# Kernel tuning notes

Hardware: AMD Instinct MI355X
Metric: run time of the kernel (lower is better)

## Reference

```python
import jax, jax.numpy as jnp
import numpy as np
from jax import lax

K_SIZE = 3
STRIDE = 1
PAD = 1
BN_EPS = 1e-5


def _unfold(x, k, stride, pad):
    # x: [B, C, H, W] -> patches [B, L, C*k*k] with torch.unfold feature
    # ordering (channel-major: feat = c*k*k + i*k + j), L = oH*oW
    B, C, H, W = x.shape
    xp = jnp.pad(x, ((0, 0), (0, 0), (pad, pad), (pad, pad)))
    oH = (H + 2 * pad - k) // stride + 1
    oW = (W + 2 * pad - k) // stride + 1
    views = []
    for i in range(k):
        for j in range(k):
            views.append(xp[:, :, i:i + oH * stride:stride, j:j + oW * stride:stride])
    p = jnp.stack(views, axis=0)            # [k*k, B, C, oH, oW]
    p = p.transpose(1, 3, 4, 2, 0)          # [B, oH, oW, C, k*k]
    return p.reshape(B, oH * oW, C * k * k), oH, oW


def _nearest_l1(flat, cents):
    # Online nearest-centroid search under L1, avoids [N, K] x D blowup.
    # flat: [N, D], cents: [K, D] -> int32 indices [N] (first min on ties,
    # matching torch argmin)
    N = flat.shape[0]
    init = (jnp.full((N,), jnp.inf, flat.dtype), jnp.zeros((N,), jnp.int32))
    ks = jnp.arange(cents.shape[0], dtype=jnp.int32)

    def body(carry, kc):
        kidx, c = kc
        d = jnp.abs(flat - c).sum(-1)       # [N]
        bd, bi = carry
        better = d < bd
        return (jnp.where(better, d, bd), jnp.where(better, kidx, bi)), None

    (_, best_idx), _ = lax.scan(body, init, (ks, cents))
    return best_idx


def setup_inputs() -> dict:
    key = jax.random.key(0)
    ks = jax.random.split(key, 5)
    B, Cin, H, W = 8, 64, 56, 56
    K, D, Cout = 256, Cin * K_SIZE * K_SIZE, 128
    return {
        "x": jax.random.normal(ks[0], (B, Cin, H, W), jnp.float32),
        "centroids": jax.random.normal(ks[1], (K, D), jnp.float32),
        "residual_centroids": jax.random.normal(ks[2], (K, D), jnp.float32),
        "dot_centroids": jax.random.normal(ks[3], (K, Cout), jnp.float32),
        "dot_residual_centroids": jax.random.normal(ks[4], (K, Cout), jnp.float32),
        "bn_gamma": jnp.ones((Cout,), jnp.float32),
        "bn_beta": jnp.zeros((Cout,), jnp.float32),
    }


def reference(x, centroids, residual_centroids, dot_centroids,
              dot_residual_centroids, bn_gamma, bn_beta):
    B = x.shape[0]
    Cout = dot_centroids.shape[1]
    patches, oH, oW = _unfold(x, K_SIZE, STRIDE, PAD)   # [B, L, D]
    L, D = patches.shape[1], patches.shape[2]
    flat = patches.reshape(B * L, D)

    # Stage 1: nearest centroid (L1)
    idx1 = _nearest_l1(flat, centroids)                  # [B*L]
    residuals = flat - centroids[idx1]                   # [B*L, D]
    # Stage 2: nearest residual centroid (L1)
    idx2 = _nearest_l1(residuals, residual_centroids)    # [B*L]

    # LUT gather + sum
    out_vals = dot_centroids[idx1] + dot_residual_centroids[idx2]  # [B*L, Cout]
    out = out_vals.reshape(B, L, Cout).transpose(0, 2, 1).reshape(B, Cout, oH, oW)

    # BatchNorm2d (training mode: biased batch statistics)
    mean = out.mean(axis=(0, 2, 3), keepdims=True)
    var = ((out - mean) ** 2).mean(axis=(0, 2, 3), keepdims=True)
    out = (out - mean) * lax.rsqrt(var + BN_EPS)
    out = out * bn_gamma[None, :, None, None] + bn_beta[None, :, None, None]
    return out
```

## Files before the change

### kernel.cpp

```cpp
#include <hip/hip_runtime.h>

#define NP 25088
#define DD 576
#define KC 256

__global__ __launch_bounds__(256) void unfold_kernel(const float* __restrict__ x,
                                                     float* __restrict__ PT) {
  const int d = blockIdx.y;
  const int n = blockIdx.x * 256 + threadIdx.x;
  const int c = d / 9, r = d % 9;
  const int di = r / 3 - 1, dj = r % 3 - 1;
  const int b = n / 3136, hw = n % 3136;
  const int h = hw / 56 + di, w = hw % 56 + dj;
  float v = 0.0f;
  if (h >= 0 && h < 56 && w >= 0 && w < 56)
    v = x[(((size_t)b * 64 + c) * 56 + h) * 56 + w];
  PT[(size_t)d * NP + n] = v;
}

__global__ __launch_bounds__(256) void transpose_kernel(const float* __restrict__ C,
                                                        float* __restrict__ CT) {
  const int d = blockIdx.x;
  const int k = threadIdx.x;
  CT[d * KC + k] = C[k * DD + d];
}

__global__ __launch_bounds__(256, 3) void nearest_kernel(const float* __restrict__ AT,
                                                         const float* __restrict__ CT,
                                                         float* __restrict__ distc,
                                                         int* __restrict__ idxc) {
  __shared__ float As[2][32][64];
  __shared__ float Bs[2][32][128];

  const int tid = threadIdx.x;
  const int tm = tid >> 4;
  const int tk = tid & 15;
  const int m0 = blockIdx.x * 64;
  const int kc = blockIdx.y;

  float part[4][8], tot[4][8];
  float4 ra[2], rb[4];

#define LOADT(ch) do {                                                              \
    _Pragma("unroll")                                                               \
    for (int q = 0; q < 2; ++q) {                                                   \
      int f = q * 256 + tid;                                                        \
      ra[q] = *(const float4*)(AT + (size_t)((ch) * 32 + (f >> 4)) * NP + m0 +      \
                               (f & 15) * 4);                                       \
    }                                                                               \
    _Pragma("unroll")                                                               \
    for (int q = 0; q < 4; ++q) {                                                   \
      int f = q * 256 + tid;                                                        \
      rb[q] = *(const float4*)(CT + (size_t)((ch) * 32 + (f >> 5)) * KC +           \
                               kc * 128 + (f & 31) * 4);                            \
    }                                                                               \
  } while (0)

#define WRITET(bf) do {                                                             \
    _Pragma("unroll")                                                               \
    for (int q = 0; q < 2; ++q) {                                                   \
      int f = q * 256 + tid;                                                        \
      *(float4*)&As[bf][f >> 4][(f & 15) * 4] = ra[q];                              \
    }                                                                               \
    _Pragma("unroll")                                                               \
    for (int q = 0; q < 4; ++q) {                                                   \
      int f = q * 256 + tid;                                                        \
      *(float4*)&Bs[bf][f >> 5][(f & 31) * 4] = rb[q];                              \
    }                                                                               \
  } while (0)

  LOADT(0);
  WRITET(0);
#pragma unroll
  for (int i = 0; i < 4; ++i)
#pragma unroll
    for (int j = 0; j < 8; ++j) tot[i][j] = 0.0f;

  for (int ch = 0; ch < 18; ++ch) {
    if ((ch & 1) == 0) {
#pragma unroll
      for (int i = 0; i < 4; ++i)
#pragma unroll
        for (int j = 0; j < 8; ++j) part[i][j] = 0.0f;
    }
    __syncthreads();
    if (ch < 17) LOADT(ch + 1);
    const int buf = ch & 1;
#pragma unroll 4
    for (int d = 0; d < 32; ++d) {
      float a[4], b[8];
      *(float4*)&a[0] = *(const float4*)&As[buf][d][tm * 4];
      *(float4*)&b[0] = *(const float4*)&Bs[buf][d][tk * 4];
      *(float4*)&b[4] = *(const float4*)&Bs[buf][d][64 + tk * 4];
#pragma unroll
      for (int i = 0; i < 4; ++i)
#pragma unroll
        for (int j = 0; j < 8; ++j) part[i][j] += fabsf(a[i] - b[j]);
    }
    if (ch < 17) WRITET((ch + 1) & 1);
    if (ch & 1) {
#pragma unroll
      for (int i = 0; i < 4; ++i)
#pragma unroll
        for (int j = 0; j < 8; ++j) tot[i][j] += part[i][j];
    }
  }

#pragma unroll
  for (int i = 0; i < 4; ++i) {
    float bd = tot[i][0];
    int bk = kc * 128 + tk * 4;
#pragma unroll
    for (int j = 1; j < 8; ++j) {
      int kk = kc * 128 + (j < 4 ? tk * 4 + j : 64 + tk * 4 + (j - 4));
      if (tot[i][j] < bd) { bd = tot[i][j]; bk = kk; }
    }
#pragma unroll
    for (int off = 1; off < 16; off <<= 1) {
      float od = __shfl_xor(bd, off, 64);
      int ok = __shfl_xor(bk, off, 64);
      if (od < bd || (od == bd && ok < bk)) { bd = od; bk = ok; }
    }
    if (tk == 0) {
      const int m = m0 + tm * 4 + i;
      distc[(size_t)kc * NP + m] = bd;
      idxc[(size_t)kc * NP + m] = bk;
    }
  }
#undef LOADT
#undef WRITET
}

__global__ __launch_bounds__(256) void combine_kernel(const float* __restrict__ distc,
                                                      const int* __restrict__ idxc,
                                                      int* __restrict__ idx_out) {
  const int n = blockIdx.x * 256 + threadIdx.x;
  if (n >= NP) return;
  const float d0 = distc[n], d1 = distc[NP + n];
  idx_out[n] = (d1 < d0) ? idxc[NP + n] : idxc[n];
}

__global__ __launch_bounds__(256) void resid_kernel(float* __restrict__ PT,
                                                    const float* __restrict__ C1T,
                                                    const int* __restrict__ idx1) {
  const int d = blockIdx.y;
  const int n = blockIdx.x * 256 + threadIdx.x;
  const int k = idx1[n];
  PT[(size_t)d * NP + n] -= C1T[d * KC + k];
}

__global__ __launch_bounds__(256) void stats_kernel(const int* __restrict__ idx1,
                                                    const int* __restrict__ idx2,
                                                    const float* __restrict__ dotc,
                                                    const float* __restrict__ dotrc,
                                                    float* __restrict__ gsum,
                                                    float* __restrict__ gsq) {
  __shared__ float ssum[4][128], ssq[4][128];
  const int tid = threadIdx.x, lane = tid & 63, wv = tid >> 6;
  const int wid = blockIdx.x * 4 + wv;
  float s0 = 0.f, s1 = 0.f, q0 = 0.f, q1 = 0.f;
  for (int n = wid; n < NP; n += 512) {
    const int k1 = idx1[n], k2 = idx2[n];
    const float2 u = ((const float2*)(dotc + (size_t)k1 * 128))[lane];
    const float2 v = ((const float2*)(dotrc + (size_t)k2 * 128))[lane];
    const float x0 = u.x + v.x, x1 = u.y + v.y;
    s0 += x0; s1 += x1; q0 += x0 * x0; q1 += x1 * x1;
  }
  ssum[wv][lane * 2] = s0; ssum[wv][lane * 2 + 1] = s1;
  ssq[wv][lane * 2] = q0;  ssq[wv][lane * 2 + 1] = q1;
  __syncthreads();
  if (tid < 128) {
    const float s = ssum[0][tid] + ssum[1][tid] + ssum[2][tid] + ssum[3][tid];
    const float q = ssq[0][tid] + ssq[1][tid] + ssq[2][tid] + ssq[3][tid];
    atomicAdd(&gsum[tid], s);
    atomicAdd(&gsq[tid], q);
  }
}

__global__ void finalize_kernel(const float* __restrict__ gsum,
                                const float* __restrict__ gsq,
                                const float* __restrict__ gamma,
                                const float* __restrict__ beta,
                                float* __restrict__ scalev,
                                float* __restrict__ shiftv) {
  const int c = threadIdx.x;
  const float mean = gsum[c] * (1.0f / NP);
  const float var = gsq[c] * (1.0f / NP) - mean * mean;
  const float inv = rsqrtf(var + 1e-5f);
  const float sc = gamma[c] * inv;
  scalev[c] = sc;
  shiftv[c] = beta[c] - mean * sc;
}

__global__ __launch_bounds__(256) void output_kernel(const int* __restrict__ idx1,
                                                     const int* __restrict__ idx2,
                                                     const float* __restrict__ dotc,
                                                     const float* __restrict__ dotrc,
                                                     const float* __restrict__ scalev,
                                                     const float* __restrict__ shiftv,
                                                     float* __restrict__ out) {
  __shared__ float vals[64][128];
  const int tid = threadIdx.x, lane = tid & 63, wv = tid >> 6;
  const int blk = blockIdx.x;
  const int b = blk / 49, hw0 = (blk % 49) * 64;
  const int n0 = b * 3136 + hw0;
  const float sc0 = scalev[lane * 2], sc1 = scalev[lane * 2 + 1];
  const float sh0 = shiftv[lane * 2], sh1 = shiftv[lane * 2 + 1];
  for (int t = 0; t < 16; ++t) {
    const int nn = wv * 16 + t;
    const int n = n0 + nn;
    const int k1 = idx1[n], k2 = idx2[n];
    const float2 u = ((const float2*)(dotc + (size_t)k1 * 128))[lane];
    const float2 v = ((const float2*)(dotrc + (size_t)k2 * 128))[lane];
    *(float2*)&vals[nn][lane * 2] =
        make_float2(sc0 * (u.x + v.x) + sh0, sc1 * (u.y + v.y) + sh1);
  }
  __syncthreads();
  const int c = tid >> 1, half = tid & 1;
  float* op = out + ((size_t)b * 128 + c) * 3136 + hw0 + half * 32;
#pragma unroll
  for (int i = 0; i < 32; i += 4) {
    float4 w4;
    w4.x = vals[half * 32 + i + 0][c];
    w4.y = vals[half * 32 + i + 1][c];
    w4.z = vals[half * 32 + i + 2][c];
    w4.w = vals[half * 32 + i + 3][c];
    *(float4*)(op + i) = w4;
  }
}

extern "C" void kernel_launch(void* const* d_in, const int* in_sizes, int n_in,
                              void* d_out, int out_size, void* d_ws, size_t ws_size,
                              hipStream_t stream) {
  const float* x     = (const float*)d_in[0];
  const float* cent  = (const float*)d_in[1];
  const float* rcent = (const float*)d_in[2];
  const float* dotc  = (const float*)d_in[3];
  const float* dotrc = (const float*)d_in[4];
  const float* gamma = (const float*)d_in[5];
  const float* beta  = (const float*)d_in[6];
  float* out = (float*)d_out;

  float* PT  = (float*)d_ws;
  float* C1T = PT + (size_t)DD * NP;
  float* C2T = C1T + (size_t)DD * KC;
  int* idx1  = (int*)(C2T + (size_t)DD * KC);
  int* idx2  = idx1 + NP;
  float* distc = (float*)(idx2 + NP);
  int* idxc    = (int*)(distc + 2 * NP);
  float* gsum   = (float*)(idxc + 2 * NP);
  float* gsq    = gsum + 128;
  float* scalev = gsq + 128;
  float* shiftv = scalev + 128;

  unfold_kernel<<<dim3(98, 576), 256, 0, stream>>>(x, PT);
  transpose_kernel<<<576, 256, 0, stream>>>(cent, C1T);
  transpose_kernel<<<576, 256, 0, stream>>>(rcent, C2T);
  nearest_kernel<<<dim3(392, 2), 256, 0, stream>>>(PT, C1T, distc, idxc);
  combine_kernel<<<98, 256, 0, stream>>>(distc, idxc, idx1);
  resid_kernel<<<dim3(98, 576), 256, 0, stream>>>(PT, C1T, idx1);
  nearest_kernel<<<dim3(392, 2), 256, 0, stream>>>(PT, C2T, distc, idxc);
  combine_kernel<<<98, 256, 0, stream>>>(distc, idxc, idx2);
  hipMemsetAsync(gsum, 0, 256 * sizeof(float), stream);
  stats_kernel<<<128, 256, 0, stream>>>(idx1, idx2, dotc, dotrc, gsum, gsq);
  finalize_kernel<<<1, 128, 0, stream>>>(gsum, gsq, gamma, beta, scalev, shiftv);
  output_kernel<<<392, 256, 0, stream>>>(idx1, idx2, dotc, dotrc, scalev, shiftv, out);
}
```

Measured before the change: 737.0 us.

## Shrink nearest-centroid tile to 64x64, split K four ways with XCD-aware mapping

The L1 nearest-centroid kernel now uses 64x64 tiles (4x4 per thread) instead of 64x128, and splits the centroid dimension into four chunks. The launch grid is a flat 1568 blocks whose index is remapped so that blocks on the same XCD share point tiles, and occupancy is raised to 5 blocks per CU. The combine kernel now reduces four partial results instead of two. This trades lower register pressure and more parallelism for reduced arithmetic intensity per shared-memory load and more A-tile reloads from global memory.

```diff
diff --git a/kernel.cpp b/kernel.cpp
--- a/kernel.cpp
+++ b/kernel.cpp
@@ -25,100 +25,87 @@
   CT[d * KC + k] = C[k * DD + d];
 }
 
-__global__ __launch_bounds__(256, 3) void nearest_kernel(const float* __restrict__ AT,
+#define ACC4(p, a, s) \
+  do { p.x += fabsf(a.x - (s)); p.y += fabsf(a.y - (s)); \
+       p.z += fabsf(a.z - (s)); p.w += fabsf(a.w - (s)); } while (0)
+#define ADD4(t, p) \
+  do { t.x += p.x; t.y += p.y; t.z += p.z; t.w += p.w; } while (0)
+#define COMP(v, i) ((i) == 0 ? (v).x : (i) == 1 ? (v).y : (i) == 2 ? (v).z : (v).w)
+
+__global__ __launch_bounds__(256, 5) void nearest_kernel(const float* __restrict__ AT,
                                                          const float* __restrict__ CT,
                                                          float* __restrict__ distc,
                                                          int* __restrict__ idxc) {
   __shared__ float As[2][32][64];
-  __shared__ float Bs[2][32][128];
+  __shared__ float Bs[2][32][64];
 
   const int tid = threadIdx.x;
   const int tm = tid >> 4;
   const int tk = tid & 15;
-  const int m0 = blockIdx.x * 64;
-  const int kc = blockIdx.y;
-
-  float part[4][8], tot[4][8];
-  float4 ra[2], rb[4];
-
-#define LOADT(ch) do {                                                              \
-    _Pragma("unroll")                                                               \
-    for (int q = 0; q < 2; ++q) {                                                   \
-      int f = q * 256 + tid;                                                        \
-      ra[q] = *(const float4*)(AT + (size_t)((ch) * 32 + (f >> 4)) * NP + m0 +      \
-                               (f & 15) * 4);                                       \
-    }                                                                               \
-    _Pragma("unroll")                                                               \
-    for (int q = 0; q < 4; ++q) {                                                   \
-      int f = q * 256 + tid;                                                        \
-      rb[q] = *(const float4*)(CT + (size_t)((ch) * 32 + (f >> 5)) * KC +           \
-                               kc * 128 + (f & 31) * 4);                            \
-    }                                                                               \
+  const int L = blockIdx.x;
+  const int xcd = L & 7, r = L >> 3;
+  const int mb = xcd * 49 + (r >> 2);
+  const int kc = r & 3;
+  const int m0 = mb * 64, k0 = kc * 64;
+
+  float4 ra0, ra1, rb0, rb1;
+  float4 p0, p1, p2, p3, t0, t1, t2, t3;
+
+  const int frow = tid >> 4, fcol = (tid & 15) * 4;
+  const float* ap = AT + (size_t)frow * NP + m0 + fcol;
+  const float* bp = CT + frow * KC + k0 + fcol;
+
+#define LOADT() do {                                       \
+    ra0 = *(const float4*)(ap);                            \
+    ra1 = *(const float4*)(ap + (size_t)16 * NP);          \
+    rb0 = *(const float4*)(bp);                            \
+    rb1 = *(const float4*)(bp + 16 * KC);                  \
+    ap += (size_t)32 * NP; bp += 32 * KC;                  \
   } while (0)
 
-#define WRITET(bf) do {                                                             \
-    _Pragma("unroll")                                                               \
-    for (int q = 0; q < 2; ++q) {                                                   \
-      int f = q * 256 + tid;                                                        \
-      *(float4*)&As[bf][f >> 4][(f & 15) * 4] = ra[q];                              \
-    }                                                                               \
-    _Pragma("unroll")                                                               \
-    for (int q = 0; q < 4; ++q) {                                                   \
-      int f = q * 256 + tid;                                                        \
-      *(float4*)&Bs[bf][f >> 5][(f & 31) * 4] = rb[q];                              \
-    }                                                                               \
+#define WRITET(bf) do {                                    \
+    *(float4*)&As[bf][frow][fcol] = ra0;                   \
+    *(float4*)&As[bf][16 + frow][fcol] = ra1;              \
+    *(float4*)&Bs[bf][frow][fcol] = rb0;                   \
+    *(float4*)&Bs[bf][16 + frow][fcol] = rb1;              \
   } while (0)
 
-  LOADT(0);
+  LOADT();
   WRITET(0);
-#pragma unroll
-  for (int i = 0; i < 4; ++i)
-#pragma unroll
-    for (int j = 0; j < 8; ++j) tot[i][j] = 0.0f;
+  t0 = t1 = t2 = t3 = make_float4(0.f, 0.f, 0.f, 0.f);
 
   for (int ch = 0; ch < 18; ++ch) {
-    if ((ch & 1) == 0) {
-#pragma unroll
-      for (int i = 0; i < 4; ++i)
-#pragma unroll
-        for (int j = 0; j < 8; ++j) part[i][j] = 0.0f;
-    }
+    if ((ch & 1) == 0) p0 = p1 = p2 = p3 = make_float4(0.f, 0.f, 0.f, 0.f);
     __syncthreads();
-    if (ch < 17) LOADT(ch + 1);
+    if (ch < 17) LOADT();
     const int buf = ch & 1;
-#pragma unroll 4
+#pragma unroll 8
     for (int d = 0; d < 32; ++d) {
-      float a[4], b[8];
-      *(float4*)&a[0] = *(const float4*)&As[buf][d][tm * 4];
-      *(float4*)&b[0] = *(const float4*)&Bs[buf][d][tk * 4];
-      *(float4*)&b[4] = *(const float4*)&Bs[buf][d][64 + tk * 4];
-#pragma unroll
-      for (int i = 0; i < 4; ++i)
-#pragma unroll
-        for (int j = 0; j < 8; ++j) part[i][j] += fabsf(a[i] - b[j]);
+      const float4 a = *(const float4*)&As[buf][d][tm * 4];
+      const float4 b = *(const float4*)&Bs[buf][d][tk * 4];
+      ACC4(p0, a, b.x);
+      ACC4(p1, a, b.y);
+      ACC4(p2, a, b.z);
+      ACC4(p3, a, b.w);
     }
     if (ch < 17) WRITET((ch + 1) & 1);
     if (ch & 1) {
-#pragma unroll
-      for (int i = 0; i < 4; ++i)
-#pragma unroll
-        for (int j = 0; j < 8; ++j) tot[i][j] += part[i][j];
+      ADD4(t0, p0); ADD4(t1, p1); ADD4(t2, p2); ADD4(t3, p3);
     }
   }
 
 #pragma unroll
   for (int i = 0; i < 4; ++i) {
-    float bd = tot[i][0];
-    int bk = kc * 128 + tk * 4;
-#pragma unroll
-    for (int j = 1; j < 8; ++j) {
-      int kk = kc * 128 + (j < 4 ? tk * 4 + j : 64 + tk * 4 + (j - 4));
-      if (tot[i][j] < bd) { bd = tot[i][j]; bk = kk; }
-    }
+    const float d0 = COMP(t0, i), d1 = COMP(t1, i), d2 = COMP(t2, i), d3 = COMP(t3, i);
+    float bd = d0;
+    int bk = k0 + tk * 4;
+    if (d1 < bd) { bd = d1; bk = k0 + tk * 4 + 1; }
+    if (d2 < bd) { bd = d2; bk = k0 + tk * 4 + 2; }
+    if (d3 < bd) { bd = d3; bk = k0 + tk * 4 + 3; }
 #pragma unroll
     for (int off = 1; off < 16; off <<= 1) {
-      float od = __shfl_xor(bd, off, 64);
-      int ok = __shfl_xor(bk, off, 64);
+      const float od = __shfl_xor(bd, off, 64);
+      const int ok = __shfl_xor(bk, off, 64);
       if (od < bd || (od == bd && ok < bk)) { bd = od; bk = ok; }
     }
     if (tk == 0) {
@@ -136,8 +123,14 @@
                                                       int* __restrict__ idx_out) {
   const int n = blockIdx.x * 256 + threadIdx.x;
   if (n >= NP) return;
-  const float d0 = distc[n], d1 = distc[NP + n];
-  idx_out[n] = (d1 < d0) ? idxc[NP + n] : idxc[n];
+  float bd = distc[n];
+  int bi = idxc[n];
+#pragma unroll
+  for (int s = 1; s < 4; ++s) {
+    const float d = distc[(size_t)s * NP + n];
+    if (d < bd) { bd = d; bi = idxc[(size_t)s * NP + n]; }
+  }
+  idx_out[n] = bi;
 }
 
 __global__ __launch_bounds__(256) void resid_kernel(float* __restrict__ PT,
@@ -247,8 +240,8 @@
   int* idx1  = (int*)(C2T + (size_t)DD * KC);
   int* idx2  = idx1 + NP;
   float* distc = (float*)(idx2 + NP);
-  int* idxc    = (int*)(distc + 2 * NP);
-  float* gsum   = (float*)(idxc + 2 * NP);
+  int* idxc    = (int*)(distc + 4 * NP);
+  float* gsum   = (float*)(idxc + 4 * NP);
   float* gsq    = gsum + 128;
   float* scalev = gsq + 128;
   float* shiftv = scalev + 128;
@@ -256,10 +249,10 @@
   unfold_kernel<<<dim3(98, 576), 256, 0, stream>>>(x, PT);
   transpose_kernel<<<576, 256, 0, stream>>>(cent, C1T);
   transpose_kernel<<<576, 256, 0, stream>>>(rcent, C2T);
-  nearest_kernel<<<dim3(392, 2), 256, 0, stream>>>(PT, C1T, distc, idxc);
+  nearest_kernel<<<1568, 256, 0, stream>>>(PT, C1T, distc, idxc);
   combine_kernel<<<98, 256, 0, stream>>>(distc, idxc, idx1);
   resid_kernel<<<dim3(98, 576), 256, 0, stream>>>(PT, C1T, idx1);
-  nearest_kernel<<<dim3(392, 2), 256, 0, stream>>>(PT, C2T, distc, idxc);
+  nearest_kernel<<<1568, 256, 0, stream>>>(PT, C2T, distc, idxc);
   combine_kernel<<<98, 256, 0, stream>>>(distc, idxc, idx2);
   hipMemsetAsync(gsum, 0, 256 * sizeof(float), stream);
   stats_kernel<<<128, 256, 0, stream>>>(idx1, idx2, dotc, dotrc, gsum, gsq);
```

Result: faster. 589.7 us (-20.0%).
